# Kernel optimization log

Hardware: AMD Instinct MI355X
Metric: run time of the kernel (lower is better)

The kernel has to match this reference:

```python
import jax, jax.numpy as jnp
import numpy as np

B, N = 8, 1024
NFEAT, NHID, NHEADS, NCLASS, NLAYERS = 256, 64, 8, 256, 2
ALPHA = 0.2  # LeakyReLU slope inside GAT layers
OUTER_SLOPE = 0.01  # F.leaky_relu default on concatenated heads
NEG = -9e15


def setup_inputs() -> dict:
    key = jax.random.key(0)
    ks = jax.random.split(key, 8)
    x = jax.random.normal(ks[0], (B, N, NFEAT), jnp.float32)
    adj = jax.random.randint(ks[1], (B, N, N), 0, 2).astype(jnp.int32)
    mask = jax.random.randint(ks[2], (B, N), 0, 2).astype(jnp.int32)
    W_att = (jax.random.normal(ks[3], (NHEADS, NFEAT, NHID), jnp.float32) * 0.05)
    a_att = (jax.random.normal(ks[4], (NHEADS, 2 * NHID), jnp.float32) * 0.05)
    W_out = (jax.random.normal(ks[5], (NHID * NHEADS, NCLASS), jnp.float32) * 0.05)
    a_out = (jax.random.normal(ks[6], (2 * NCLASS,), jnp.float32) * 0.05)
    ln_w = jnp.ones((NCLASS,), jnp.float32)
    ln_b = jnp.zeros((NCLASS,), jnp.float32)
    return {"x": x, "adj": adj, "mask": mask, "W_att": W_att, "a_att": a_att,
            "W_out": W_out, "a_out": a_out, "ln_w": ln_w, "ln_b": ln_b}


def _layernorm(x, w, b):
    mu = jnp.mean(x, axis=-1, keepdims=True)
    var = jnp.mean(jnp.square(x - mu), axis=-1, keepdims=True)
    return (x - mu) * jax.lax.rsqrt(var + 1e-5) * w + b


def _gat_forward(x, adj_pos, maskb, W_att, a_att, W_out, a_out, ln_w, ln_b):
    for _ in range(NLAYERS):
        # multi-head GAT layers (concat=True): e_ij = leakyrelu(f1_i + f2_j)
        h = jnp.einsum('bnf,hfo->bhno', x, W_att)            # [B,H,N,F]
        f1 = jnp.einsum('bhno,ho->bhn', h, a_att[:, :NHID])  # [B,H,N]
        f2 = jnp.einsum('bhno,ho->bhn', h, a_att[:, NHID:])
        e = jax.nn.leaky_relu(f1[:, :, :, None] + f2[:, :, None, :], ALPHA)
        att = jax.nn.softmax(jnp.where(adj_pos[:, None], e, NEG), axis=-1)
        hp = jax.nn.elu(jnp.einsum('bhnm,bhmo->bhno', att, h))
        y = jax.nn.leaky_relu(
            hp.transpose(0, 2, 1, 3).reshape(B, N, NHEADS * NHID), OUTER_SLOPE)
        # out attention layer (concat=False)
        ho = y @ W_out                                        # [B,N,C]
        g1 = ho @ a_out[:NCLASS]                              # [B,N]
        g2 = ho @ a_out[NCLASS:]
        eo = jax.nn.leaky_relu(g1[:, :, None] + g2[:, None, :], ALPHA)
        ao = jax.nn.softmax(jnp.where(adj_pos, eo, NEG), axis=-1)
        x = x + jax.nn.elu(jnp.einsum('bnm,bmo->bno', ao, ho))
        x = jnp.where(maskb, 0.0, x)
        x = _layernorm(x, ln_w, ln_b)
    return jax.nn.relu(x), jax.nn.relu(x[:, 0, :])


def reference(x, adj, mask, W_att, a_att, W_out, a_out, ln_w, ln_b):
    adj_pos = adj > 0
    maskb = (mask == 0)[:, :, None]
    return _gat_forward(x, adj_pos, maskb, W_att, a_att, W_out, a_out, ln_w, ln_b)
```

## Files before the change

kernel.cpp:

```cpp
#include <hip/hip_runtime.h>
#include <hip/hip_bf16.h>
#include <math.h>

#define BB 8
#define NN 1024
#define FF 256
#define HH 8
#define OO 64
#define CC 256

typedef __attribute__((ext_vector_type(8))) short short8;
typedef __attribute__((ext_vector_type(4))) short s16x4;
typedef __attribute__((ext_vector_type(4))) float f32x4;
typedef unsigned long long u64;

__device__ __forceinline__ short bf16s(float f) {
    __hip_bfloat16 h = __float2bfloat16(f);
    return *reinterpret_cast<short*>(&h);
}

__global__ void k_adjprep(const int* __restrict__ adj, u64* __restrict__ adjbit) {
    int i = blockIdx.x * 256 + threadIdx.x;
    u64 m = __ballot(adj[i] > 0);
    if ((threadIdx.x & 63) == 0) adjbit[i >> 6] = m;
}

__global__ void k_wprep(const float* __restrict__ Wa, const float* __restrict__ Wo,
                        __hip_bfloat16* __restrict__ WaT, __hip_bfloat16* __restrict__ WoT) {
    int i = blockIdx.x * 256 + threadIdx.x;
    if (i < 131072) {
        int hd = i >> 14, o = (i >> 8) & 63, f = i & 255;
        WaT[i] = __float2bfloat16(Wa[hd * 16384 + f * 64 + o]);
    } else {
        int j = i - 131072;
        int c = j >> 9, k = j & 511;
        WoT[j] = __float2bfloat16(Wo[k * 256 + c]);
    }
}

__global__ void k_proj_mfma(const float* __restrict__ x,
                            const __hip_bfloat16* __restrict__ WaT,
                            const float* __restrict__ aatt,
                            __hip_bfloat16* __restrict__ hF,
                            float* __restrict__ f1, float* __restrict__ f2) {
    int tile = blockIdx.x, hd = blockIdx.y;
    int t = threadIdx.x, lane = t & 63, w = t >> 6;
    int r0 = tile * 64;
    int b = r0 >> 10;
    int n0 = r0 & 1023;
    int bh = b * HH + hd;
    int al = lane & 15, ah = lane >> 4;
    const float* xrow = x + (size_t)(r0 + w * 16 + al) * FF;
    const __hip_bfloat16* Wb = WaT + (size_t)hd * OO * FF;
    f32x4 z4 = {0.f, 0.f, 0.f, 0.f};
    f32x4 acc[4] = {z4, z4, z4, z4};
    for (int k0 = 0; k0 < FF; k0 += 32) {
        int k = k0 + ah * 8;
        short8 af;
#pragma unroll
        for (int q = 0; q < 8; ++q) af[q] = bf16s(xrow[k + q]);
#pragma unroll
        for (int cf = 0; cf < 4; ++cf) {
            int col = cf * 16 + al;
            short8 bf = *(const short8*)&Wb[(size_t)col * FF + k];
            acc[cf] = __builtin_amdgcn_mfma_f32_16x16x32_bf16(af, bf, acc[cf], 0, 0, 0);
        }
    }
    int kw = tile & 15;
    int half = w >> 1;
    int hg = (w & 1) * 2 + (ah >> 1);
    int q0 = (ah & 1) * 4;
#pragma unroll
    for (int cf = 0; cf < 4; ++cf) {
        size_t base = ((((size_t)bh * 16 + kw) * 4 + cf) * 2 + half) * 512 +
                      (hg * 16 + al) * 8 + q0;
        s16x4 v;
#pragma unroll
        for (int r = 0; r < 4; ++r) v[r] = bf16s(acc[cf][r]);
        *(s16x4*)&hF[base] = v;
    }
    int nb = n0 + w * 16 + ah * 4;
    float p1[4] = {0.f, 0.f, 0.f, 0.f}, p2[4] = {0.f, 0.f, 0.f, 0.f};
#pragma unroll
    for (int cf = 0; cf < 4; ++cf) {
        int col = cf * 16 + al;
        float a1 = aatt[hd * 2 * OO + col];
        float a2 = aatt[hd * 2 * OO + OO + col];
#pragma unroll
        for (int r = 0; r < 4; ++r) {
            p1[r] += acc[cf][r] * a1;
            p2[r] += acc[cf][r] * a2;
        }
    }
#pragma unroll
    for (int off = 1; off < 16; off <<= 1) {
#pragma unroll
        for (int r = 0; r < 4; ++r) {
            p1[r] += __shfl_xor(p1[r], off);
            p2[r] += __shfl_xor(p2[r], off);
        }
    }
    if (al == 0) {
#pragma unroll
        for (int r = 0; r < 4; ++r) {
            f1[(size_t)bh * NN + nb + r] = p1[r];
            f2[(size_t)bh * NN + nb + r] = p2[r];
        }
    }
}

__global__ void k_att_fused(const u64* __restrict__ adjbit, const float* __restrict__ f1,
                            const float* __restrict__ f2,
                            const __hip_bfloat16* __restrict__ hF,
                            __hip_bfloat16* __restrict__ ybf) {
    int orig = blockIdx.x;
    int wgid = (orig & 7) * 128 + (orig >> 3);
    int bh = wgid >> 4;
    int n0 = (wgid & 15) * 64;
    int b = bh >> 3, hd = bh & 7;
    int t = threadIdx.x, lane = t & 63, w = t >> 6;
    __shared__ float Qs[1024], Ss[1024];
    __shared__ u64 bits[64 * 17];
    const float* f2b = f2 + (size_t)bh * NN;
    for (int j = t; j < 1024; j += 256) {
        float v = f2b[j];
        Qs[j] = __expf(v);
        Ss[j] = __expf(0.2f * v);
    }
    for (int e = t; e < 1024; e += 256) {
        int rr = e >> 4, c = e & 15;
        bits[rr * 17 + c] = adjbit[((size_t)b * NN + n0 + rr) * 16 + c];
    }
    int g = lane >> 4, r = lane & 15;
    int row = w * 16 + r;
    float fl = f1[(size_t)bh * NN + n0 + row];
    float P = __expf(fl), R = __expf(0.2f * fl);
    __syncthreads();
    const __hip_bfloat16* hFb = hF + (size_t)bh * 16 * 4 * 2 * 512 + lane * 8;
    f32x4 z4 = {0.f, 0.f, 0.f, 0.f};
    f32x4 acc[4] = {z4, z4, z4, z4};
    float ps = 0.f;
    int c0 = g * 8;
#pragma unroll 2
    for (int k0 = 0; k0 < NN; k0 += 64) {
        int kw = k0 >> 6;
        u64 m = bits[row * 17 + kw];
        unsigned bl0 = (unsigned)(m >> c0) & 0xffu;
        unsigned bl1 = (unsigned)(m >> (32 + c0)) & 0xffu;
        f32x4 qa0 = *(const f32x4*)&Qs[k0 + c0];
        f32x4 qb0 = *(const f32x4*)&Qs[k0 + c0 + 4];
        f32x4 sa0 = *(const f32x4*)&Ss[k0 + c0];
        f32x4 sb0 = *(const f32x4*)&Ss[k0 + c0 + 4];
        f32x4 qa1 = *(const f32x4*)&Qs[k0 + 32 + c0];
        f32x4 qb1 = *(const f32x4*)&Qs[k0 + 32 + c0 + 4];
        f32x4 sa1 = *(const f32x4*)&Ss[k0 + 32 + c0];
        f32x4 sb1 = *(const f32x4*)&Ss[k0 + 32 + c0 + 4];
        short8 a0, a1;
#pragma unroll
        for (int e = 0; e < 4; ++e) {
            float v0 = ((bl0 >> e) & 1) ? fmaxf(P * qa0[e], R * sa0[e]) : 0.f;
            float v1 = ((bl0 >> (4 + e)) & 1) ? fmaxf(P * qb0[e], R * sb0[e]) : 0.f;
            float v2 = ((bl1 >> e) & 1) ? fmaxf(P * qa1[e], R * sa1[e]) : 0.f;
            float v3 = ((bl1 >> (4 + e)) & 1) ? fmaxf(P * qb1[e], R * sb1[e]) : 0.f;
            ps += (v0 + v1) + (v2 + v3);
            a0[e] = bf16s(v0);
            a0[4 + e] = bf16s(v1);
            a1[e] = bf16s(v2);
            a1[4 + e] = bf16s(v3);
        }
#pragma unroll
        for (int cf = 0; cf < 4; ++cf) {
            const __hip_bfloat16* blk = hFb + ((size_t)(kw * 4 + cf) * 2) * 512;
            short8 b0 = *(const short8*)&blk[0];
            short8 b1 = *(const short8*)&blk[512];
            acc[cf] = __builtin_amdgcn_mfma_f32_16x16x32_bf16(a0, b0, acc[cf], 0, 0, 0);
            acc[cf] = __builtin_amdgcn_mfma_f32_16x16x32_bf16(a1, b1, acc[cf], 0, 0, 0);
        }
    }
    ps += __shfl_xor(ps, 16);
    ps += __shfl_xor(ps, 32);
#pragma unroll
    for (int rr = 0; rr < 4; ++rr) {
        int rloc = g * 4 + rr;
        float dn = __shfl(ps, rloc);
        float ids = 1.0f / dn;
        int nrow = n0 + w * 16 + rloc;
#pragma unroll
        for (int cf = 0; cf < 4; ++cf) {
            float v = acc[cf][rr] * ids;
            float e = v > 0.f ? v : expm1f(v);
            float yv = e > 0.f ? e : 0.01f * e;
            ybf[((size_t)b * NN + nrow) * 512 + hd * OO + cf * 16 + r] =
                __float2bfloat16(yv);
        }
    }
}

__global__ void k_outproj_mfma(const __hip_bfloat16* __restrict__ ybf,
                               const __hip_bfloat16* __restrict__ WoT,
                               const float* __restrict__ ao,
                               __hip_bfloat16* __restrict__ hoF,
                               float* __restrict__ g1, float* __restrict__ g2) {
    int tile = blockIdx.x;
    int t = threadIdx.x, lane = t & 63, w = t >> 6;
    int r0 = tile * 32;
    int b = r0 >> 10;
    __shared__ __align__(16) __hip_bfloat16 As[32][520];
    __shared__ float pg1[4][32], pg2[4][32];
    for (int e = t; e < 2048; e += 256) {
        int row = e >> 6, k8 = (e & 63) * 8;
        *(short8*)&As[row][k8] = *(const short8*)&ybf[(size_t)(r0 + row) * 512 + k8];
    }
    __syncthreads();
    int al = lane & 15, ah = lane >> 4;
    f32x4 z4 = {0.f, 0.f, 0.f, 0.f};
    f32x4 acc0[4] = {z4, z4, z4, z4};
    f32x4 acc1[4] = {z4, z4, z4, z4};
    for (int k0 = 0; k0 < 512; k0 += 32) {
        int k = k0 + ah * 8;
        short8 a0 = *(const short8*)&As[al][k];
        short8 a1 = *(const short8*)&As[16 + al][k];
#pragma unroll
        for (int cf = 0; cf < 4; ++cf) {
            int col = w * 64 + cf * 16 + al;
            short8 bf = *(const short8*)&WoT[(size_t)col * 512 + k];
            acc0[cf] = __builtin_amdgcn_mfma_f32_16x16x32_bf16(a0, bf, acc0[cf], 0, 0, 0);
            acc1[cf] = __builtin_amdgcn_mfma_f32_16x16x32_bf16(a1, bf, acc1[cf], 0, 0, 0);
        }
    }
    int kw = (tile >> 1) & 15;
    int half = tile & 1;
    int hg0 = ah >> 1;
    int q0 = (ah & 1) * 4;
    float q1[8] = {0.f, 0.f, 0.f, 0.f, 0.f, 0.f, 0.f, 0.f};
    float q2[8] = {0.f, 0.f, 0.f, 0.f, 0.f, 0.f, 0.f, 0.f};
#pragma unroll
    for (int cf = 0; cf < 4; ++cf) {
        int col = w * 64 + cf * 16 + al;
        int cfB = w * 4 + cf;
        float a1v = ao[col], a2v = ao[CC + col];
        size_t base = ((((size_t)b * 16 + kw) * 16 + cfB) * 2 + half) * 512;
        s16x4 v0, v1;
#pragma unroll
        for (int r = 0; r < 4; ++r) {
            v0[r] = bf16s(acc0[cf][r]);
            v1[r] = bf16s(acc1[cf][r]);
            q1[r] += acc0[cf][r] * a1v;
            q2[r] += acc0[cf][r] * a2v;
            q1[4 + r] += acc1[cf][r] * a1v;
            q2[4 + r] += acc1[cf][r] * a2v;
        }
        *(s16x4*)&hoF[base + (hg0 * 16 + al) * 8 + q0] = v0;
        *(s16x4*)&hoF[base + ((hg0 + 2) * 16 + al) * 8 + q0] = v1;
    }
#pragma unroll
    for (int off = 1; off < 16; off <<= 1) {
#pragma unroll
        for (int j = 0; j < 8; ++j) {
            q1[j] += __shfl_xor(q1[j], off);
            q2[j] += __shfl_xor(q2[j], off);
        }
    }
    if (al == 0) {
#pragma unroll
        for (int j = 0; j < 8; ++j) {
            int row = (j >> 2) * 16 + ah * 4 + (j & 3);
            pg1[w][row] = q1[j];
            pg2[w][row] = q2[j];
        }
    }
    __syncthreads();
    if (t < 32) {
        g1[r0 + t] = pg1[0][t] + pg1[1][t] + pg1[2][t] + pg1[3][t];
        g2[r0 + t] = pg2[0][t] + pg2[1][t] + pg2[2][t] + pg2[3][t];
    }
}

__global__ void k_out_fused(const u64* __restrict__ adjbit, const float* __restrict__ g1,
                            const float* __restrict__ g2,
                            const __hip_bfloat16* __restrict__ hoF,
                            const float* __restrict__ xin, float* __restrict__ tout) {
    int orig = blockIdx.x;
    int wgid = (orig & 7) * 64 + (orig >> 3);
    int b = wgid >> 6;
    int n0 = (wgid & 63) * 16;
    int t = threadIdx.x, lane = t & 63, w = t >> 6;
    __shared__ float Qs[1024], Ss[1024];
    __shared__ u64 bits[16 * 17];
    __shared__ __align__(16) __hip_bfloat16 As[16][264];
    __shared__ float psum[4][16];
    const float* g2b = g2 + (size_t)b * NN;
    for (int j = t; j < 1024; j += 256) {
        float v = g2b[j];
        Qs[j] = __expf(v);
        Ss[j] = __expf(0.2f * v);
    }
    {
        int rr = t >> 4, c = t & 15;
        bits[rr * 17 + c] = adjbit[((size_t)b * NN + n0 + rr) * 16 + c];
    }
    int br = t & 15, kg = t >> 4;
    float gl = g1[(size_t)b * NN + n0 + br];
    float P = __expf(gl);
    float R = __expf(0.2f * gl);
    int ar = lane & 15, g = lane >> 4;
    const __hip_bfloat16* hoFb = hoF + (size_t)b * 16 * 16 * 2 * 512 + lane * 8;
    f32x4 z4 = {0.f, 0.f, 0.f, 0.f};
    f32x4 acc[4] = {z4, z4, z4, z4};
    float ps = 0.f;
    __syncthreads();
    for (int ks = 0; ks < NN; ks += 256) {
        u64 m = bits[br * 17 + (ks >> 6) + (kg >> 2)];
        int sh = (kg & 3) * 16;
        short8 vv[2];
#pragma unroll
        for (int h = 0; h < 2; ++h) {
            short8 vx;
#pragma unroll
            for (int e4 = 0; e4 < 2; ++e4) {
                int cw = kg * 16 + h * 8 + e4 * 4;
                f32x4 q4 = *(const f32x4*)&Qs[ks + cw];
                f32x4 s4 = *(const f32x4*)&Ss[ks + cw];
#pragma unroll
                for (int e = 0; e < 4; ++e) {
                    float val = ((m >> (sh + h * 8 + e4 * 4 + e)) & 1)
                                    ? fmaxf(P * q4[e], R * s4[e]) : 0.f;
                    ps += val;
                    vx[e4 * 4 + e] = bf16s(val);
                }
            }
            vv[h] = vx;
        }
        *(short8*)&As[br][kg * 16] = vv[0];
        *(short8*)&As[br][kg * 16 + 8] = vv[1];
        __syncthreads();
#pragma unroll
        for (int ksub = 0; ksub < 4; ++ksub) {
            int kw = (ks >> 6) + ksub;
            short8 a0 = *(const short8*)&As[ar][ksub * 64 + g * 8];
            short8 a1 = *(const short8*)&As[ar][ksub * 64 + 32 + g * 8];
#pragma unroll
            for (int cf = 0; cf < 4; ++cf) {
                int cfB = w * 4 + cf;
                const __hip_bfloat16* blk = hoFb + ((size_t)(kw * 16 + cfB) * 2) * 512;
                short8 b0 = *(const short8*)&blk[0];
                short8 b1 = *(const short8*)&blk[512];
                acc[cf] = __builtin_amdgcn_mfma_f32_16x16x32_bf16(a0, b0, acc[cf], 0, 0, 0);
                acc[cf] = __builtin_amdgcn_mfma_f32_16x16x32_bf16(a1, b1, acc[cf], 0, 0, 0);
            }
        }
        __syncthreads();
    }
    ps += __shfl_xor(ps, 16);
    ps += __shfl_xor(ps, 32);
    if (lane < 16) psum[w][lane] = ps;
    __syncthreads();
#pragma unroll
    for (int rr = 0; rr < 4; ++rr) {
        int rloc = g * 4 + rr;
        float dn = psum[0][rloc] + psum[1][rloc] + psum[2][rloc] + psum[3][rloc];
        float ids = 1.0f / dn;
        size_t rowo = ((size_t)b * NN + n0 + rloc) * CC;
#pragma unroll
        for (int cf = 0; cf < 4; ++cf) {
            int col = w * 64 + cf * 16 + ar;
            float v = acc[cf][rr] * ids;
            float e = v > 0.f ? v : expm1f(v);
            tout[rowo + col] = xin[rowo + col] + e;
        }
    }
}

__global__ void k_mask_ln(const float* __restrict__ tin, const int* __restrict__ mask,
                          const float* __restrict__ lw, const float* __restrict__ lb,
                          float* __restrict__ xout, float* __restrict__ outf, int final_) {
    int n = blockIdx.x, b = blockIdx.y, t = threadIdx.x;
    int lane = t & 63, w = t >> 6;
    float v = (mask[b * NN + n] == 0) ? 0.f : tin[((size_t)b * NN + n) * CC + t];
    __shared__ float r1[4], r2[4];
    float s = v;
    for (int off = 32; off; off >>= 1) s += __shfl_xor(s, off);
    if (lane == 0) r1[w] = s;
    __syncthreads();
    float mu = (r1[0] + r1[1] + r1[2] + r1[3]) * (1.0f / CC);
    float d = v - mu;
    float q = d * d;
    for (int off = 32; off; off >>= 1) q += __shfl_xor(q, off);
    if (lane == 0) r2[w] = q;
    __syncthreads();
    float var = (r2[0] + r2[1] + r2[2] + r2[3]) * (1.0f / CC);
    float ln = d * rsqrtf(var + 1e-5f) * lw[t] + lb[t];
    size_t idx = ((size_t)b * NN + n) * CC + t;
    if (final_) {
        float rv = ln > 0.f ? ln : 0.f;
        outf[idx] = rv;
        if (n == 0) outf[(size_t)BB * NN * CC + b * CC + t] = rv;
    } else {
        xout[idx] = ln;
    }
}

extern "C" void kernel_launch(void* const* d_in, const int* in_sizes, int n_in,
                              void* d_out, int out_size, void* d_ws, size_t ws_size,
                              hipStream_t stream) {
    const float* x = (const float*)d_in[0];
    const int* adj = (const int*)d_in[1];
    const int* mask = (const int*)d_in[2];
    const float* W_att = (const float*)d_in[3];
    const float* a_att = (const float*)d_in[4];
    const float* W_out = (const float*)d_in[5];
    const float* a_out = (const float*)d_in[6];
    const float* ln_w = (const float*)d_in[7];
    const float* ln_b = (const float*)d_in[8];
    float* out = (float*)d_out;

    float* ws = (float*)d_ws;
    float* xbuf = ws;
    float* tbuf = xbuf + 2097152;
    float* f1   = tbuf + 2097152;
    float* f2   = f1 + 65536;
    float* g1   = f2 + 65536;
    float* g2   = g1 + 8192;
    float* p    = g2 + 8192;
    __hip_bfloat16* hF  = (__hip_bfloat16*)p;
    __hip_bfloat16* ybf = (__hip_bfloat16*)(p + 2097152);
    __hip_bfloat16* hoF = (__hip_bfloat16*)(p + 4194304);
    __hip_bfloat16* WaT = (__hip_bfloat16*)(p + 5242880);
    __hip_bfloat16* WoT = (__hip_bfloat16*)(p + 5308416);
    u64* adjbit = (u64*)(p + 5373952);

    k_wprep<<<1024, 256, 0, stream>>>(W_att, W_out, WaT, WoT);
    k_adjprep<<<32768, 256, 0, stream>>>(adj, adjbit);

    for (int layer = 0; layer < 2; ++layer) {
        const float* xin_l = layer ? xbuf : x;
        k_proj_mfma<<<dim3(128, 8), 256, 0, stream>>>(xin_l, WaT, a_att, hF, f1, f2);
        k_att_fused<<<1024, 256, 0, stream>>>(adjbit, f1, f2, hF, ybf);
        k_outproj_mfma<<<256, 256, 0, stream>>>(ybf, WoT, a_out, hoF, g1, g2);
        k_out_fused<<<512, 256, 0, stream>>>(adjbit, g1, g2, hoF, xin_l, tbuf);
        k_mask_ln<<<dim3(NN, BB), 256, 0, stream>>>(tbuf, mask, ln_w, ln_b, xbuf, out,
                                                    layer == 1);
    }
}
```

Measured before the change: 239.3 us.

## Fuse mask+LayerNorm into output attention kernel and feed bf16 x to projection

Removes the separate mask/LayerNorm kernel by computing row sums and sums of squares inside the output attention kernel, reducing across lanes and waves via shared memory, then writing the normalized result directly. The fused kernel also writes a bf16 copy of x, and a new prep kernel converts the initial input to bf16. The projection kernel can then load short8 vectors instead of converting fp32 element by element. This drops a full fp32 write and read of the intermediate tensor and one launch per layer, but variance is now computed as E[x^2]-mu^2, which is less numerically stable.

```diff
diff --git a/kernel.cpp b/kernel.cpp
--- a/kernel.cpp
+++ b/kernel.cpp
@@ -17,6 +17,11 @@
 __device__ __forceinline__ short bf16s(float f) {
     __hip_bfloat16 h = __float2bfloat16(f);
     return *reinterpret_cast<short*>(&h);
+}
+
+__global__ void k_xprep(const float* __restrict__ x, __hip_bfloat16* __restrict__ xbf) {
+    int i = blockIdx.x * 256 + threadIdx.x;
+    xbf[i] = __float2bfloat16(x[i]);
 }
 
 __global__ void k_adjprep(const int* __restrict__ adj, u64* __restrict__ adjbit) {
@@ -38,7 +43,7 @@
     }
 }
 
-__global__ void k_proj_mfma(const float* __restrict__ x,
+__global__ void k_proj_mfma(const __hip_bfloat16* __restrict__ xbf,
                             const __hip_bfloat16* __restrict__ WaT,
                             const float* __restrict__ aatt,
                             __hip_bfloat16* __restrict__ hF,
@@ -50,15 +55,13 @@
     int n0 = r0 & 1023;
     int bh = b * HH + hd;
     int al = lane & 15, ah = lane >> 4;
-    const float* xrow = x + (size_t)(r0 + w * 16 + al) * FF;
+    const __hip_bfloat16* xrow = xbf + (size_t)(r0 + w * 16 + al) * FF;
     const __hip_bfloat16* Wb = WaT + (size_t)hd * OO * FF;
     f32x4 z4 = {0.f, 0.f, 0.f, 0.f};
     f32x4 acc[4] = {z4, z4, z4, z4};
     for (int k0 = 0; k0 < FF; k0 += 32) {
         int k = k0 + ah * 8;
-        short8 af;
-#pragma unroll
-        for (int q = 0; q < 8; ++q) af[q] = bf16s(xrow[k + q]);
+        short8 af = *(const short8*)&xrow[k];
 #pragma unroll
         for (int cf = 0; cf < 4; ++cf) {
             int col = cf * 16 + al;
@@ -279,7 +282,10 @@
 __global__ void k_out_fused(const u64* __restrict__ adjbit, const float* __restrict__ g1,
                             const float* __restrict__ g2,
                             const __hip_bfloat16* __restrict__ hoF,
-                            const float* __restrict__ xin, float* __restrict__ tout) {
+                            const float* __restrict__ xin, const int* __restrict__ mask,
+                            const float* __restrict__ lw, const float* __restrict__ lb,
+                            float* __restrict__ xout, __hip_bfloat16* __restrict__ xbfout,
+                            float* __restrict__ outf, int final_) {
     int orig = blockIdx.x;
     int wgid = (orig & 7) * 64 + (orig >> 3);
     int b = wgid >> 6;
@@ -289,6 +295,7 @@
     __shared__ u64 bits[16 * 17];
     __shared__ __align__(16) __hip_bfloat16 As[16][264];
     __shared__ float psum[4][16];
+    __shared__ float lns[4][16], lnq[4][16];
     const float* g2b = g2 + (size_t)b * NN;
     for (int j = t; j < 1024; j += 256) {
         float v = g2b[j];
@@ -355,48 +362,60 @@
     ps += __shfl_xor(ps, 32);
     if (lane < 16) psum[w][lane] = ps;
     __syncthreads();
+    float tv[4][4];
 #pragma unroll
     for (int rr = 0; rr < 4; ++rr) {
         int rloc = g * 4 + rr;
         float dn = psum[0][rloc] + psum[1][rloc] + psum[2][rloc] + psum[3][rloc];
         float ids = 1.0f / dn;
-        size_t rowo = ((size_t)b * NN + n0 + rloc) * CC;
+        int nrow = n0 + rloc;
+        int mk = mask[b * NN + nrow];
+        size_t rowo = ((size_t)b * NN + nrow) * CC;
+        float s1 = 0.f, s2 = 0.f;
 #pragma unroll
         for (int cf = 0; cf < 4; ++cf) {
             int col = w * 64 + cf * 16 + ar;
             float v = acc[cf][rr] * ids;
             float e = v > 0.f ? v : expm1f(v);
-            tout[rowo + col] = xin[rowo + col] + e;
-        }
-    }
-}
-
-__global__ void k_mask_ln(const float* __restrict__ tin, const int* __restrict__ mask,
-                          const float* __restrict__ lw, const float* __restrict__ lb,
-                          float* __restrict__ xout, float* __restrict__ outf, int final_) {
-    int n = blockIdx.x, b = blockIdx.y, t = threadIdx.x;
-    int lane = t & 63, w = t >> 6;
-    float v = (mask[b * NN + n] == 0) ? 0.f : tin[((size_t)b * NN + n) * CC + t];
-    __shared__ float r1[4], r2[4];
-    float s = v;
-    for (int off = 32; off; off >>= 1) s += __shfl_xor(s, off);
-    if (lane == 0) r1[w] = s;
-    __syncthreads();
-    float mu = (r1[0] + r1[1] + r1[2] + r1[3]) * (1.0f / CC);
-    float d = v - mu;
-    float q = d * d;
-    for (int off = 32; off; off >>= 1) q += __shfl_xor(q, off);
-    if (lane == 0) r2[w] = q;
-    __syncthreads();
-    float var = (r2[0] + r2[1] + r2[2] + r2[3]) * (1.0f / CC);
-    float ln = d * rsqrtf(var + 1e-5f) * lw[t] + lb[t];
-    size_t idx = ((size_t)b * NN + n) * CC + t;
-    if (final_) {
-        float rv = ln > 0.f ? ln : 0.f;
-        outf[idx] = rv;
-        if (n == 0) outf[(size_t)BB * NN * CC + b * CC + t] = rv;
-    } else {
-        xout[idx] = ln;
+            float tvv = (mk == 0) ? 0.f : (xin[rowo + col] + e);
+            tv[rr][cf] = tvv;
+            s1 += tvv;
+            s2 += tvv * tvv;
+        }
+#pragma unroll
+        for (int off = 1; off < 16; off <<= 1) {
+            s1 += __shfl_xor(s1, off);
+            s2 += __shfl_xor(s2, off);
+        }
+        if (ar == 0) {
+            lns[w][rloc] = s1;
+            lnq[w][rloc] = s2;
+        }
+    }
+    __syncthreads();
+#pragma unroll
+    for (int rr = 0; rr < 4; ++rr) {
+        int rloc = g * 4 + rr;
+        int nrow = n0 + rloc;
+        size_t rowo = ((size_t)b * NN + nrow) * CC;
+        float su = lns[0][rloc] + lns[1][rloc] + lns[2][rloc] + lns[3][rloc];
+        float sq = lnq[0][rloc] + lnq[1][rloc] + lnq[2][rloc] + lnq[3][rloc];
+        float mu = su * (1.0f / CC);
+        float var = sq * (1.0f / CC) - mu * mu;
+        float rstd = rsqrtf(var + 1e-5f);
+#pragma unroll
+        for (int cf = 0; cf < 4; ++cf) {
+            int col = w * 64 + cf * 16 + ar;
+            float ln = (tv[rr][cf] - mu) * rstd * lw[col] + lb[col];
+            if (final_) {
+                float rv = ln > 0.f ? ln : 0.f;
+                outf[rowo + col] = rv;
+                if (nrow == 0) outf[(size_t)BB * NN * CC + b * CC + col] = rv;
+            } else {
+                xout[rowo + col] = ln;
+                xbfout[rowo + col] = __float2bfloat16(ln);
+            }
+        }
     }
 }
 
@@ -416,12 +435,13 @@
 
     float* ws = (float*)d_ws;
     float* xbuf = ws;
-    float* tbuf = xbuf + 2097152;
-    float* f1   = tbuf + 2097152;
+    float* xbfr = xbuf + 2097152;
+    float* f1   = xbfr + 2097152;
     float* f2   = f1 + 65536;
     float* g1   = f2 + 65536;
     float* g2   = g1 + 8192;
     float* p    = g2 + 8192;
+    __hip_bfloat16* xbf = (__hip_bfloat16*)xbfr;
     __hip_bfloat16* hF  = (__hip_bfloat16*)p;
     __hip_bfloat16* ybf = (__hip_bfloat16*)(p + 2097152);
     __hip_bfloat16* hoF = (__hip_bfloat16*)(p + 4194304);
@@ -431,14 +451,14 @@
 
     k_wprep<<<1024, 256, 0, stream>>>(W_att, W_out, WaT, WoT);
     k_adjprep<<<32768, 256, 0, stream>>>(adj, adjbit);
+    k_xprep<<<8192, 256, 0, stream>>>(x, xbf);
 
     for (int layer = 0; layer < 2; ++layer) {
         const float* xin_l = layer ? xbuf : x;
-        k_proj_mfma<<<dim3(128, 8), 256, 0, stream>>>(xin_l, WaT, a_att, hF, f1, f2);
+        k_proj_mfma<<<dim3(128, 8), 256, 0, stream>>>(xbf, WaT, a_att, hF, f1, f2);
         k_att_fused<<<1024, 256, 0, stream>>>(adjbit, f1, f2, hF, ybf);
         k_outproj_mfma<<<256, 256, 0, stream>>>(ybf, WoT, a_out, hoF, g1, g2);
-        k_out_fused<<<512, 256, 0, stream>>>(adjbit, g1, g2, hoF, xin_l, tbuf);
-        k_mask_ln<<<dim3(NN, BB), 256, 0, stream>>>(tbuf, mask, ln_w, ln_b, xbuf, out,
-                                                    layer == 1);
-    }
-}
+        k_out_fused<<<512, 256, 0, stream>>>(adjbit, g1, g2, hoF, xin_l, mask,
+                                             ln_w, ln_b, xbuf, xbf, out, layer == 1);
+    }
+}
```

New measurement: 226.4 us. 1.06x faster.
